# Optimization experiments

Measured on AMD Instinct MI355X. Metric: run time of the kernel, lower is better.

## Reference

```python
import jax, jax.numpy as jnp
import numpy as np
from jax import lax

H = 256          # hidden_size
VOCAB = 30000
N_OPS = 9
N_COLS = 16
T = 4            # num_time_steps
Q = 64           # question length
N_NUM = 8        # numbers appearing in the question
ROWS = 1_000_000

# operation indices (Neural Programmer, ICLR 2016 op set)
OP_SUM, OP_COUNT, OP_DIFF, OP_GREATER, OP_LESSER, OP_AND, OP_OR, OP_ASSIGN, OP_RESET = range(N_OPS)


def setup_inputs() -> dict:
    key = jax.random.key(0)
    ks = jax.random.split(key, 13)
    s = 0.05
    f32 = jnp.float32
    return {
        "input_question": jax.random.randint(ks[0], (Q,), 0, VOCAB),
        "input_question_numbers": jax.random.randint(ks[1], (N_NUM,), 0, 100),
        "left_word_indices": jax.random.randint(ks[2], (N_NUM,), 0, Q),
        "table": jax.random.normal(ks[3], (ROWS, N_COLS), f32),
        # learned parameters
        "emb": jax.random.normal(ks[4], (VOCAB, H), f32) * s,      # question word embeddings
        "Wx": jax.random.normal(ks[5], (H, H), f32) * s,           # question RNN input weight
        "Wh": jax.random.normal(ks[6], (H, H), f32) * s,           # question RNN recurrent weight
        "W_op": jax.random.normal(ks[7], (H, 2 * H), f32) * s,     # selector (op branch)
        "op_emb": jax.random.normal(ks[8], (N_OPS, H), f32) * s,   # operation embeddings
        "W_col": jax.random.normal(ks[9], (H, 2 * H), f32) * s,    # selector (column branch)
        "col_emb": jax.random.normal(ks[10], (N_COLS, H), f32) * s,# column embeddings
        "W_hist": jax.random.normal(ks[11], (H, 3 * H), f32) * s,  # history RNN
        "U": jax.random.normal(ks[12], (2, H), f32) * s,           # lesser/greater pivot vectors
    }


def reference(input_question, input_question_numbers, left_word_indices, table,
              emb, Wx, Wh, W_op, op_emb, W_col, col_emb, W_hist, U):
    dt = table.dtype
    hid = Wx.shape[0]

    # ---- question RNN (simple tanh RNN) ----
    xs = emb[input_question]                               # [Q, H]
    def step(h, x):
        h2 = jnp.tanh(x @ Wx.T + h @ Wh.T)
        return h2, h2
    q, hs = lax.scan(step, jnp.zeros((hid,), dt), xs)      # q=[H], hs=[Q,H]

    # ---- pivot computation (z_matrix = hidden states left of each number) ----
    z = hs[left_word_indices]                              # [N_NUM, H]
    nums = input_question_numbers.astype(dt)               # [N_NUM]
    l_pivot = jax.nn.softmax(z @ U[0]) @ nums              # scalar
    g_pivot = jax.nn.softmax(z @ U[1]) @ nums              # scalar

    # soft comparison maps (pivots are timestep-independent; compute once)
    sel_l = jax.nn.sigmoid(l_pivot - table)                # [R, C] ~ [table < l_pivot]
    sel_g = jax.nn.sigmoid(table - g_pivot)                # [R, C] ~ [table > g_pivot]

    h_hist = jnp.zeros((hid,), dt)
    scalars = [jnp.zeros((), dt)]
    rs_list = [jnp.ones((table.shape[0],), dt)]
    lookup = jnp.zeros(table.shape, dt)

    for _ in range(T):
        rs1 = rs_list[-1]
        rs2 = rs_list[max(0, len(rs_list) - 2)]
        s1 = scalars[-1]
        s3 = scalars[max(0, len(scalars) - 3)]

        # selector: soft op / column distributions from [question; history]
        qh = jnp.concatenate([q, h_hist])                  # [2H]
        a_op = jax.nn.softmax(op_emb @ jnp.tanh(W_op @ qh))    # [N_OPS]
        a_col = jax.nn.softmax(col_emb @ jnp.tanh(W_col @ qh)) # [N_COLS]

        # row select (soft mixture over ops)
        rs = (a_op[OP_GREATER] * (sel_g @ a_col)
              + a_op[OP_LESSER] * (sel_l @ a_col)
              + a_op[OP_AND] * jnp.minimum(rs1, rs2)
              + a_op[OP_OR] * jnp.maximum(rs1, rs2)
              + a_op[OP_RESET] * jnp.ones_like(rs1)
              + (a_op[OP_SUM] + a_op[OP_COUNT] + a_op[OP_DIFF] + a_op[OP_ASSIGN]) * rs1)

        # scalar answer
        scalar = (a_op[OP_SUM] * jnp.sum(rs1 @ table)
                  + a_op[OP_COUNT] * jnp.sum(rs1)
                  + a_op[OP_DIFF] * (s3 - s1))

        # lookup answer: assign op prints selected rows/columns
        lookup = a_op[OP_ASSIGN] * rs[:, None] * a_col[None, :]

        # history RNN
        c = jnp.concatenate([a_op @ op_emb, a_col @ col_emb, h_hist])  # [3H]
        h_hist = jnp.tanh(W_hist @ c)

        rs_list.append(rs)
        scalars.append(scalar)

    return scalars[-1], lookup
```

## Files before the change

### kernel.cpp

```cpp
#include <hip/hip_runtime.h>
#include <hip/hip_fp16.h>
#include <math.h>

#define HDIM   256
#define QLEN   64
#define NNUM   8
#define NOPS   9
#define NCOLS  16
#define TSTEPS 4


#define WS_LPIV 0
#define WS_GPIV 1
#define WS_ACOL 2
#define WS_AOP  66
#define WS_Q    112
#define WS_PQO  368
#define WS_PQC  624
#define WS_HS   880
#define WS_XP   2928
#define WS_AH   19312
#define WS_BH   21616
#define WS_WH16 25712
#define WS_M16  58480
#define WS_PART 156784
#define NBLK_C  2048
#define PRE2_BLOCKS 409

typedef _Float16 f16x8 __attribute__((ext_vector_type(8)));
typedef _Float16 f16x4 __attribute__((ext_vector_type(4)));
typedef float    f32x4 __attribute__((ext_vector_type(4)));

__device__ __forceinline__ float fast_tanh(float x) {
    return 1.0f - 2.0f / (__expf(2.0f * x) + 1.0f);
}

__global__ void precompute_kernel(const int* __restrict__ q,
                                  const float* __restrict__ emb,
                                  const float* __restrict__ Wx,
                                  const float* __restrict__ Wh,
                                  float* __restrict__ ws) {
    int gid = blockIdx.x * 256 + threadIdx.x;
    if (gid < QLEN * HDIM) {
        int t = gid >> 8, j = gid & 255;
        const float4* x4 = (const float4*)(emb + (size_t)q[t] * HDIM);
        const float4* w4 = (const float4*)(Wx + (size_t)j * HDIM);
        float s = 0.f;
        for (int k = 0; k < HDIM / 4; k++) {
            float4 a = x4[k], b = w4[k];
            s += a.x * b.x + a.y * b.y + a.z * b.z + a.w * b.w;
        }
        ws[WS_XP + t * HDIM + j] = s;
    } else {
        int did = gid - QLEN * HDIM;
        int hidx = did * 2;
        int e = hidx & 7, qr = (hidx >> 3) & 15, quad = (hidx >> 7) & 3;
        int kk = (hidx >> 9) & 7, t = hidx >> 12;
        const float* src = Wh + (size_t)(16 * t + qr) * HDIM + kk * 32 + quad * 8 + e;
        float2 v = *(const float2*)src;
        ((__half2*)(ws + WS_WH16))[did] = __floats2half2_rn(v.x, v.y);
    }
}

__global__ __launch_bounds__(256, 1) void rnn_kernel(
        float* __restrict__ ws,
        const int* __restrict__ lwi,
        const float* __restrict__ W_op,
        const float* __restrict__ W_col,
        const float* __restrict__ W_hist,
        const float* __restrict__ op_emb,
        const float* __restrict__ col_emb,
        const float* __restrict__ table,
        int rows) {
    if (blockIdx.x >= 1 + PRE2_BLOCKS) {
        int wid = blockIdx.x - 1 - PRE2_BLOCKS;
        const f32x4* t4 = (const f32x4*)table;
        long n4 = (long)rows * (NCOLS / 4);
        f32x4 acc = {0.f, 0.f, 0.f, 0.f};
        for (long i = (long)wid * 256 + threadIdx.x; i < n4; i += (long)2048 * 256)
            acc += t4[i];
        asm volatile("" :: "v"(acc));
        return;
    }
    if (blockIdx.x != 0) {
        int gid = (blockIdx.x - 1) * 256 + threadIdx.x;
        if (gid < HDIM * NOPS) {
            int j = gid / NOPS, o = gid % NOPS;
            const float4* w4 = (const float4*)(W_hist + (size_t)j * (3 * HDIM));
            const float4* e4 = (const float4*)(op_emb + (size_t)o * HDIM);
            float s = 0.f;
            for (int k = 0; k < HDIM / 4; k++) {
                float4 a = w4[k], b = e4[k];
                s += a.x * b.x + a.y * b.y + a.z * b.z + a.w * b.w;
            }
            ws[WS_AH + gid] = s;
        } else if (gid < HDIM * NOPS + HDIM * NCOLS) {
            int idx = gid - HDIM * NOPS;
            int j = idx / NCOLS, c = idx % NCOLS;
            const float4* w4 = (const float4*)(W_hist + (size_t)j * (3 * HDIM) + HDIM);
            const float4* e4 = (const float4*)(col_emb + (size_t)c * HDIM);
            float s = 0.f;
            for (int k = 0; k < HDIM / 4; k++) {
                float4 a = w4[k], b = e4[k];
                s += a.x * b.x + a.y * b.y + a.z * b.z + a.w * b.w;
            }
            ws[WS_BH + idx] = s;
        } else if (gid < HDIM * NOPS + HDIM * NCOLS + 98304) {
            int did = gid - (HDIM * NOPS + HDIM * NCOLS);
            int mat = did >> 15;
            int hidx = (did & 32767) * 2;
            int e = hidx & 7, j = (hidx >> 3) & 255, i = hidx >> 11;
            const float* src;
            if (mat == 0)      src = W_op   + (size_t)j * (2 * HDIM) + HDIM     + i * 8 + e;
            else if (mat == 1) src = W_col  + (size_t)j * (2 * HDIM) + HDIM     + i * 8 + e;
            else               src = W_hist + (size_t)j * (3 * HDIM) + 2 * HDIM + i * 8 + e;
            float2 v = *(const float2*)src;
            ((__half2*)(ws + WS_M16))[did] = __floats2half2_rn(v.x, v.y);
        }
        return;
    }

    __shared__ float xpL[QLEN * HDIM];
    __shared__ _Float16 hF[2][HDIM];
    __shared__ unsigned stepmask[QLEN];

    const int tid = threadIdx.x;
    const int wave = tid >> 6, lane = tid & 63;
    const int quad = lane >> 4, qr = lane & 15;
    const int myrow = 64 * wave + 16 * (qr >> 2) + quad * 4 + (qr & 3);

    #pragma unroll
    for (int i = 0; i < 16; i++) {
        int idx = (i * 256 + tid) * 4;
        *(float4*)(xpL + idx) = *(const float4*)(ws + WS_XP + idx);
    }
    if (tid < QLEN) {
        unsigned m = 0;
        #pragma unroll
        for (int i = 0; i < NNUM; i++) m |= (lwi[i] == tid) ? (1u << i) : 0u;
        stepmask[tid] = m;
    }
    const _Float16* wsh = (const _Float16*)(ws + WS_WH16);
    f16x8 aW[4][8];
    #pragma unroll
    for (int r = 0; r < 4; r++)
        #pragma unroll
        for (int kk = 0; kk < 8; kk++)
            aW[r][kk] = *(const f16x8*)(wsh + ((size_t)(((4 * wave + r) * 8 + kk) * 64 + lane)) * 8);
    #pragma unroll
    for (int r = 0; r < 4; r++)
        #pragma unroll
        for (int kk = 0; kk < 8; kk++) {
            f32x4 t = __builtin_bit_cast(f32x4, aW[r][kk]);
            asm volatile("" : "+v"(t));
            aW[r][kk] = __builtin_bit_cast(f16x8, t);
        }
    hF[0][tid] = (_Float16)0.f;
    __syncthreads();

    for (int s = 0; s < QLEN; s++) {
        const _Float16* hb = hF[s & 1];
        f16x8 bfrag[8];
        #pragma unroll
        for (int kk = 0; kk < 8; kk++)
            bfrag[kk] = *(const f16x8*)(hb + kk * 32 + quad * 8);
        f32x4 acc[4];
        #pragma unroll
        for (int r = 0; r < 4; r++) acc[r] = (f32x4){0.f, 0.f, 0.f, 0.f};
        #pragma unroll
        for (int kk = 0; kk < 8; kk++)
            #pragma unroll
            for (int r = 0; r < 4; r++)
                acc[r] = __builtin_amdgcn_mfma_f32_16x16x32_f16(aW[r][kk], bfrag[kk], acc[r], 0, 0, 0);

        f32x4 t01 = (qr & 4) ? acc[1] : acc[0];
        f32x4 t23 = (qr & 4) ? acc[3] : acc[2];
        f32x4 tt  = (qr & 8) ? t23 : t01;
        float e01 = (qr & 1) ? tt.y : tt.x;
        float e23 = (qr & 1) ? tt.w : tt.z;
        float v   = (qr & 2) ? e23 : e01;

        float h = fast_tanh(v + xpL[s * HDIM + myrow]);
        hF[(s + 1) & 1][myrow] = (_Float16)h;
        unsigned m = stepmask[s];
        while (m) {
            int i = __builtin_ctz(m);
            ws[WS_HS + i * HDIM + myrow] = h;
            m &= m - 1;
        }
        if (s == QLEN - 1) ws[WS_Q + myrow] = h;
        __syncthreads();
    }
}

__global__ void qproj_kernel(const float* __restrict__ W_op,
                             const float* __restrict__ W_col,
                             float* __restrict__ ws) {
    int gid = blockIdx.x * 256 + threadIdx.x;
    int dot = gid >> 5, l = gid & 31;
    int mat = dot >> 8, j = dot & 255;
    const float* w = (mat ? W_col : W_op) + (size_t)j * (2 * HDIM) + l * 8;
    const float* qv = ws + WS_Q + l * 8;
    float4 a0 = *(const float4*)w,        a1 = *(const float4*)(w + 4);
    float4 b0 = *(const float4*)qv,       b1 = *(const float4*)(qv + 4);
    float s = a0.x * b0.x + a0.y * b0.y + a0.z * b0.z + a0.w * b0.w
            + a1.x * b1.x + a1.y * b1.y + a1.z * b1.z + a1.w * b1.w;
    s += __shfl_xor(s, 1); s += __shfl_xor(s, 2); s += __shfl_xor(s, 4);
    s += __shfl_xor(s, 8); s += __shfl_xor(s, 16);
    if (l == 0) ws[(mat ? WS_PQC : WS_PQO) + j] = s;
}

__global__ __launch_bounds__(256) void select_kernel(
        float* __restrict__ ws,
        const float* __restrict__ U,
        const int* __restrict__ nums,
        const float* __restrict__ op_emb,
        const float* __restrict__ col_emb) {
    __shared__ float zu[16];
    __shared__ float hH[HDIM];
    __shared__ float top_op[HDIM], top_col[HDIM], mh[HDIM];
    __shared__ float logits[32];
    __shared__ float aop_s[NOPS], acol_s[NCOLS];

    const int tid = threadIdx.x;

    {
        int g = tid >> 4, l = tid & 15;
        int i = g >> 1, u = g & 1;
        const float* z = ws + WS_HS + i * HDIM + l * 16;
        const float* uu = U + u * HDIM + l * 16;
        float s = 0.f;
        #pragma unroll
        for (int k = 0; k < 4; k++) {
            float4 a = *(const float4*)(z + k * 4), b = *(const float4*)(uu + k * 4);
            s += a.x * b.x + a.y * b.y + a.z * b.z + a.w * b.w;
        }
        s += __shfl_xor(s, 1); s += __shfl_xor(s, 2);
        s += __shfl_xor(s, 4); s += __shfl_xor(s, 8);
        if (l == 0) zu[g] = s;
    }
    if (tid < HDIM) hH[tid] = 0.f;
    __syncthreads();
    if (tid == 0) {
        #pragma unroll
        for (int u = 0; u < 2; u++) {
            float mx = -1e30f;
            for (int i = 0; i < NNUM; i++) mx = fmaxf(mx, zu[i * 2 + u]);
            float se = 0.f, pv = 0.f;
            for (int i = 0; i < NNUM; i++) {
                float e = __expf(zu[i * 2 + u] - mx);
                se += e;
                pv += e * (float)nums[i];
            }
            ws[u] = pv / se;
        }
    }
    __syncthreads();

    const _Float16* wsm = (const _Float16*)(ws + WS_M16);
    const float pqo = ws[WS_PQO + tid];
    const float pqc = ws[WS_PQC + tid];

    for (int t = 0; t < TSTEPS; t++) {
        float so = 0.f, sc = 0.f, sh = 0.f;
        #pragma unroll
        for (int i = 0; i < 32; i++) {
            float4 h0 = *(const float4*)(hH + i * 8);
            float4 h1 = *(const float4*)(hH + i * 8 + 4);
            f16x8 a = *(const f16x8*)(wsm + ((size_t)(0 * 32 + i) * 256 + tid) * 8);
            f16x8 b = *(const f16x8*)(wsm + ((size_t)(1 * 32 + i) * 256 + tid) * 8);
            f16x8 c = *(const f16x8*)(wsm + ((size_t)(2 * 32 + i) * 256 + tid) * 8);
            so += (float)a[0]*h0.x + (float)a[1]*h0.y + (float)a[2]*h0.z + (float)a[3]*h0.w
                + (float)a[4]*h1.x + (float)a[5]*h1.y + (float)a[6]*h1.z + (float)a[7]*h1.w;
            sc += (float)b[0]*h0.x + (float)b[1]*h0.y + (float)b[2]*h0.z + (float)b[3]*h0.w
                + (float)b[4]*h1.x + (float)b[5]*h1.y + (float)b[6]*h1.z + (float)b[7]*h1.w;
            sh += (float)c[0]*h0.x + (float)c[1]*h0.y + (float)c[2]*h0.z + (float)c[3]*h0.w
                + (float)c[4]*h1.x + (float)c[5]*h1.y + (float)c[6]*h1.z + (float)c[7]*h1.w;
        }
        top_op[tid]  = fast_tanh(pqo + so);
        top_col[tid] = fast_tanh(pqc + sc);
        mh[tid] = sh;
        __syncthreads();

        #pragma unroll
        for (int d0 = 0; d0 < 32; d0 += 8) {
            int d = d0 + (tid >> 5), l = tid & 31;
            if (d < 25) {
                float s = 0.f;
                if (d < NOPS) {
                    const float* e = op_emb + (size_t)d * HDIM;
                    #pragma unroll
                    for (int m = 0; m < 8; m++) s += e[l * 8 + m] * top_op[l * 8 + m];
                } else {
                    const float* e = col_emb + (size_t)(d - NOPS) * HDIM;
                    #pragma unroll
                    for (int m = 0; m < 8; m++) s += e[l * 8 + m] * top_col[l * 8 + m];
                }
                s += __shfl_xor(s, 1); s += __shfl_xor(s, 2); s += __shfl_xor(s, 4);
                s += __shfl_xor(s, 8); s += __shfl_xor(s, 16);
                if (l == 0) logits[d] = s;
            }
        }
        __syncthreads();
        if (tid == 0) {
            float mx = -1e30f;
            for (int o = 0; o < NOPS; o++) mx = fmaxf(mx, logits[o]);
            float se = 0.f, e[NOPS];
            for (int o = 0; o < NOPS; o++) { e[o] = __expf(logits[o] - mx); se += e[o]; }
            for (int o = 0; o < NOPS; o++) {
                float a = e[o] / se;
                aop_s[o] = a;
                ws[WS_AOP + t * NOPS + o] = a;
            }
        } else if (tid == 32) {
            float mx = -1e30f;
            for (int c = 0; c < NCOLS; c++) mx = fmaxf(mx, logits[NOPS + c]);
            float se = 0.f, e[NCOLS];
            for (int c = 0; c < NCOLS; c++) { e[c] = __expf(logits[NOPS + c] - mx); se += e[c]; }
            for (int c = 0; c < NCOLS; c++) {
                float a = e[c] / se;
                acol_s[c] = a;
                ws[WS_ACOL + t * NCOLS + c] = a;
            }
        }
        __syncthreads();
        {
            float s = mh[tid];
            const float* ah = ws + WS_AH + tid * NOPS;
            #pragma unroll
            for (int o = 0; o < NOPS; o++) s += ah[o] * aop_s[o];
            const float* bh = ws + WS_BH + tid * NCOLS;
            #pragma unroll
            for (int c = 0; c < NCOLS; c++) s += bh[c] * acol_s[c];
            float hv = fast_tanh(s);
            __syncthreads();
            hH[tid] = hv;
        }
        __syncthreads();
    }
}

__global__ __launch_bounds__(256) void table_kernel(
        const float* __restrict__ table,
        const float* __restrict__ wsc,
        float* __restrict__ wspart,
        float* __restrict__ out,
        int rows) {
    const int tid = threadIdx.x;
    const int cq = tid & 3;
    const float lpiv = wsc[WS_LPIV];
    const float gpiv = wsc[WS_GPIV];
    float4 acol4[TSTEPS];
    float wg[TSTEPS], wl[TSTEPS], wand[TSTEPS], wor[TSTEPS], wrst[TSTEPS], wpass[TSTEPS];
    #pragma unroll
    for (int t = 0; t < TSTEPS; t++) {
        acol4[t] = make_float4(wsc[WS_ACOL + t * NCOLS + cq * 4 + 0],
                               wsc[WS_ACOL + t * NCOLS + cq * 4 + 1],
                               wsc[WS_ACOL + t * NCOLS + cq * 4 + 2],
                               wsc[WS_ACOL + t * NCOLS + cq * 4 + 3]);
        wg[t]   = wsc[WS_AOP + t * NOPS + 3];
        wl[t]   = wsc[WS_AOP + t * NOPS + 4];
        wand[t] = wsc[WS_AOP + t * NOPS + 5];
        wor[t]  = wsc[WS_AOP + t * NOPS + 6];
        wrst[t] = wsc[WS_AOP + t * NOPS + 8];
        wpass[t] = wsc[WS_AOP + t * NOPS + 0] + wsc[WS_AOP + t * NOPS + 1]
                 + wsc[WS_AOP + t * NOPS + 2] + wsc[WS_AOP + t * NOPS + 7];
    }
    const float wassign = wsc[WS_AOP + 3 * NOPS + 7];

    float dAcc[TSTEPS] = {0.f, 0.f, 0.f, 0.f};
    float nAcc[TSTEPS] = {0.f, 0.f, 0.f, 0.f};
    const long rowsL = rows;

    for (long r0 = (long)blockIdx.x * 64; r0 < rowsL; r0 += (long)NBLK_C * 64) {
        long row = r0 + (tid >> 2);
        bool valid = row < rowsL;
        f32x4 tv = {0.f, 0.f, 0.f, 0.f};
        if (valid)
            tv = __builtin_nontemporal_load((const f32x4*)(table + row * NCOLS + cq * 4));
        float prs = tv.x + tv.y + tv.z + tv.w;
        float pg[4], pl[4];
        {
            float c0 = tv.x, c1 = tv.y, c2 = tv.z, c3 = tv.w;
            float sg0 = __builtin_amdgcn_rcpf(1.f + __expf(gpiv - c0));
            float sg1 = __builtin_amdgcn_rcpf(1.f + __expf(gpiv - c1));
            float sg2 = __builtin_amdgcn_rcpf(1.f + __expf(gpiv - c2));
            float sg3 = __builtin_amdgcn_rcpf(1.f + __expf(gpiv - c3));
            float sl0 = __builtin_amdgcn_rcpf(1.f + __expf(c0 - lpiv));
            float sl1 = __builtin_amdgcn_rcpf(1.f + __expf(c1 - lpiv));
            float sl2 = __builtin_amdgcn_rcpf(1.f + __expf(c2 - lpiv));
            float sl3 = __builtin_amdgcn_rcpf(1.f + __expf(c3 - lpiv));
            #pragma unroll
            for (int t = 0; t < TSTEPS; t++) {
                pg[t] = sg0 * acol4[t].x + sg1 * acol4[t].y + sg2 * acol4[t].z + sg3 * acol4[t].w;
                pl[t] = sl0 * acol4[t].x + sl1 * acol4[t].y + sl2 * acol4[t].z + sl3 * acol4[t].w;
            }
        }
        prs += __shfl_xor(prs, 1); prs += __shfl_xor(prs, 2);
        #pragma unroll
        for (int t = 0; t < TSTEPS; t++) {
            pg[t] += __shfl_xor(pg[t], 1); pg[t] += __shfl_xor(pg[t], 2);
            pl[t] += __shfl_xor(pl[t], 1); pl[t] += __shfl_xor(pl[t], 2);
        }
        float rs1 = 1.f, rs2 = 1.f;
        float vf = valid ? 1.f : 0.f;
        #pragma unroll
        for (int i = 0; i < TSTEPS; i++) {
            dAcc[i] += vf * rs1 * prs;
            nAcc[i] += vf * rs1;
            float nrs = wg[i] * pg[i] + wl[i] * pl[i]
                      + wand[i] * fminf(rs1, rs2) + wor[i] * fmaxf(rs1, rs2)
                      + wrst[i] + wpass[i] * rs1;
            rs2 = rs1;
            rs1 = nrs;
        }
        if (valid) {
            float wa = wassign * rs1;
            float* ob = out + 1 + row * NCOLS + cq * 4;
            ob[0] = wa * acol4[3].x;
            ob[1] = wa * acol4[3].y;
            ob[2] = wa * acol4[3].z;
            ob[3] = wa * acol4[3].w;
        }
    }

    #pragma unroll
    for (int i = 0; i < TSTEPS; i++) {
        #pragma unroll
        for (int off = 32; off >= 1; off >>= 1) {
            dAcc[i] += __shfl_xor(dAcc[i], off);
            nAcc[i] += __shfl_xor(nAcc[i], off);
        }
    }
    __shared__ float redl[4][8];
    int wv = tid >> 6, ln = tid & 63;
    if (ln == 0) {
        #pragma unroll
        for (int i = 0; i < TSTEPS; i++) {
            redl[wv][i] = dAcc[i];
            redl[wv][4 + i] = nAcc[i];
        }
    }
    __syncthreads();
    if (tid < 8) {
        float s = redl[0][tid] + redl[1][tid] + redl[2][tid] + redl[3][tid];
        wspart[blockIdx.x * 8 + tid] = 0.25f * s;
    }
}

__global__ void finalize_kernel(const float* __restrict__ ws, float* __restrict__ out) {
    __shared__ float red[8];
    int a = threadIdx.x >> 5, l = threadIdx.x & 31;
    float s = 0.f;
    for (int b = l; b < NBLK_C; b += 32) s += ws[WS_PART + b * 8 + a];
    s += __shfl_xor(s, 1, 32); s += __shfl_xor(s, 2, 32); s += __shfl_xor(s, 4, 32);
    s += __shfl_xor(s, 8, 32); s += __shfl_xor(s, 16, 32);
    if (l == 0) red[a] = s;
    __syncthreads();
    if (threadIdx.x == 0) {
        float Dv[4] = {red[0], red[1], red[2], red[3]};
        float Nv[4] = {red[4], red[5], red[6], red[7]};
        const float* aop = ws + WS_AOP;
        float sc[5];
        sc[0] = 0.f;
        #pragma unroll
        for (int i = 0; i < 4; i++) {
            float s1 = sc[i];
            float s3 = sc[(i >= 2) ? (i - 2) : 0];
            sc[i + 1] = aop[i * NOPS + 0] * Dv[i] + aop[i * NOPS + 1] * Nv[i]
                      + aop[i * NOPS + 2] * (s3 - s1);
        }
        out[0] = sc[4];
    }
}

extern "C" void kernel_launch(void* const* d_in, const int* in_sizes, int n_in,
                              void* d_out, int out_size, void* d_ws, size_t ws_size,
                              hipStream_t stream) {
    const int*   q       = (const int*)d_in[0];
    const int*   nums    = (const int*)d_in[1];
    const int*   lwi     = (const int*)d_in[2];
    const float* table   = (const float*)d_in[3];
    const float* emb     = (const float*)d_in[4];
    const float* Wx      = (const float*)d_in[5];
    const float* Wh      = (const float*)d_in[6];
    const float* W_op    = (const float*)d_in[7];
    const float* op_emb  = (const float*)d_in[8];
    const float* W_col   = (const float*)d_in[9];
    const float* col_emb = (const float*)d_in[10];
    const float* W_hist  = (const float*)d_in[11];
    const float* U       = (const float*)d_in[12];
    float* out = (float*)d_out;
    float* ws  = (float*)d_ws;
    int rows = in_sizes[3] / NCOLS;

    precompute_kernel<<<192, 256, 0, stream>>>(q, emb, Wx, Wh, ws);
    rnn_kernel<<<1 + PRE2_BLOCKS + 2048, 256, 0, stream>>>(
        ws, lwi, W_op, W_col, W_hist, op_emb, col_emb, table, rows);
    qproj_kernel<<<64, 256, 0, stream>>>(W_op, W_col, ws);
    select_kernel<<<1, 256, 0, stream>>>(ws, U, nums, op_emb, col_emb);
    table_kernel<<<NBLK_C, 256, 0, stream>>>(
        table, ws, ws + WS_PART, out, rows);
    finalize_kernel<<<1, 256, 0, stream>>>(ws, out);
}
```

Before: 259.4 us.

## Fuse finalize into table kernel, split RNN MFMA chain, drop nontemporal load

Three changes. The separate finalize launch is removed: each table block stores its partials atomically, and the last block to increment an atomic counter does the final reduction and scalar computation. The RNN step's MFMA accumulation is split into two independent accumulator chains to shorten the dependency chain on the serial critical path. The table load is switched from nontemporal to a normal load. Together these cut one kernel launch and some recurrent latency, in exchange for an atomic counter that must be reset each call and possibly different cache behaviour when streaming the table.

```diff
diff --git a/kernel.cpp b/kernel.cpp
--- a/kernel.cpp
+++ b/kernel.cpp
@@ -24,6 +24,7 @@
 #define WS_WH16 25712
 #define WS_M16  58480
 #define WS_PART 156784
+#define WS_CNT  173168
 #define NBLK_C  2048
 #define PRE2_BLOCKS 409
 
@@ -41,6 +42,7 @@
                                   const float* __restrict__ Wh,
                                   float* __restrict__ ws) {
     int gid = blockIdx.x * 256 + threadIdx.x;
+    if (gid == 0) *(unsigned*)(ws + WS_CNT) = 0u;
     if (gid < QLEN * HDIM) {
         int t = gid >> 8, j = gid & 255;
         const float4* x4 = (const float4*)(emb + (size_t)q[t] * HDIM);
@@ -164,14 +166,24 @@
         #pragma unroll
         for (int kk = 0; kk < 8; kk++)
             bfrag[kk] = *(const f16x8*)(hb + kk * 32 + quad * 8);
-        f32x4 acc[4];
-        #pragma unroll
-        for (int r = 0; r < 4; r++) acc[r] = (f32x4){0.f, 0.f, 0.f, 0.f};
-        #pragma unroll
-        for (int kk = 0; kk < 8; kk++)
+        f32x4 acc[4], accB[4];
+        #pragma unroll
+        for (int r = 0; r < 4; r++) {
+            acc[r]  = (f32x4){0.f, 0.f, 0.f, 0.f};
+            accB[r] = (f32x4){0.f, 0.f, 0.f, 0.f};
+        }
+        #pragma unroll
+        for (int kk = 0; kk < 4; kk++)
             #pragma unroll
             for (int r = 0; r < 4; r++)
                 acc[r] = __builtin_amdgcn_mfma_f32_16x16x32_f16(aW[r][kk], bfrag[kk], acc[r], 0, 0, 0);
+        #pragma unroll
+        for (int kk = 4; kk < 8; kk++)
+            #pragma unroll
+            for (int r = 0; r < 4; r++)
+                accB[r] = __builtin_amdgcn_mfma_f32_16x16x32_f16(aW[r][kk], bfrag[kk], accB[r], 0, 0, 0);
+        #pragma unroll
+        for (int r = 0; r < 4; r++) acc[r] += accB[r];
 
         f32x4 t01 = (qr & 4) ? acc[1] : acc[0];
         f32x4 t23 = (qr & 4) ? acc[3] : acc[2];
@@ -377,7 +389,7 @@
         bool valid = row < rowsL;
         f32x4 tv = {0.f, 0.f, 0.f, 0.f};
         if (valid)
-            tv = __builtin_nontemporal_load((const f32x4*)(table + row * NCOLS + cq * 4));
+            tv = *(const f32x4*)(table + row * NCOLS + cq * 4);
         float prs = tv.x + tv.y + tv.z + tv.w;
         float pg[4], pl[4];
         {
@@ -444,33 +456,45 @@
     __syncthreads();
     if (tid < 8) {
         float s = redl[0][tid] + redl[1][tid] + redl[2][tid] + redl[3][tid];
-        wspart[blockIdx.x * 8 + tid] = 0.25f * s;
-    }
-}
-
-__global__ void finalize_kernel(const float* __restrict__ ws, float* __restrict__ out) {
-    __shared__ float red[8];
-    int a = threadIdx.x >> 5, l = threadIdx.x & 31;
-    float s = 0.f;
-    for (int b = l; b < NBLK_C; b += 32) s += ws[WS_PART + b * 8 + a];
-    s += __shfl_xor(s, 1, 32); s += __shfl_xor(s, 2, 32); s += __shfl_xor(s, 4, 32);
-    s += __shfl_xor(s, 8, 32); s += __shfl_xor(s, 16, 32);
-    if (l == 0) red[a] = s;
+        __hip_atomic_store(&wspart[blockIdx.x * 8 + tid], 0.25f * s,
+                           __ATOMIC_RELAXED, __HIP_MEMORY_SCOPE_AGENT);
+    }
     __syncthreads();
-    if (threadIdx.x == 0) {
-        float Dv[4] = {red[0], red[1], red[2], red[3]};
-        float Nv[4] = {red[4], red[5], red[6], red[7]};
-        const float* aop = ws + WS_AOP;
-        float sc[5];
-        sc[0] = 0.f;
-        #pragma unroll
-        for (int i = 0; i < 4; i++) {
-            float s1 = sc[i];
-            float s3 = sc[(i >= 2) ? (i - 2) : 0];
-            sc[i + 1] = aop[i * NOPS + 0] * Dv[i] + aop[i * NOPS + 1] * Nv[i]
-                      + aop[i * NOPS + 2] * (s3 - s1);
-        }
-        out[0] = sc[4];
+
+    __shared__ int lastFlag;
+    if (tid == 0) {
+        unsigned* cnt = (unsigned*)(wspart + NBLK_C * 8);
+        unsigned old = __hip_atomic_fetch_add(cnt, 1u, __ATOMIC_ACQ_REL,
+                                              __HIP_MEMORY_SCOPE_AGENT);
+        lastFlag = (old == NBLK_C - 1) ? 1 : 0;
+    }
+    __syncthreads();
+    if (lastFlag) {
+        __shared__ float redF[8];
+        int a = tid >> 5, l = tid & 31;
+        float s = 0.f;
+        for (int b = l; b < NBLK_C; b += 32)
+            s += __hip_atomic_load(&wspart[b * 8 + a], __ATOMIC_RELAXED,
+                                   __HIP_MEMORY_SCOPE_AGENT);
+        s += __shfl_xor(s, 1, 32); s += __shfl_xor(s, 2, 32); s += __shfl_xor(s, 4, 32);
+        s += __shfl_xor(s, 8, 32); s += __shfl_xor(s, 16, 32);
+        if (l == 0) redF[a] = s;
+        __syncthreads();
+        if (tid == 0) {
+            float Dv[4] = {redF[0], redF[1], redF[2], redF[3]};
+            float Nv[4] = {redF[4], redF[5], redF[6], redF[7]};
+            const float* aop = wsc + WS_AOP;
+            float sc[5];
+            sc[0] = 0.f;
+            #pragma unroll
+            for (int i = 0; i < 4; i++) {
+                float s1 = sc[i];
+                float s3 = sc[(i >= 2) ? (i - 2) : 0];
+                sc[i + 1] = aop[i * NOPS + 0] * Dv[i] + aop[i * NOPS + 1] * Nv[i]
+                          + aop[i * NOPS + 2] * (s3 - s1);
+            }
+            out[0] = sc[4];
+        }
     }
 }
 
@@ -501,5 +525,4 @@
     select_kernel<<<1, 256, 0, stream>>>(ws, U, nums, op_emb, col_emb);
     table_kernel<<<NBLK_C, 256, 0, stream>>>(
         table, ws, ws + WS_PART, out, rows);
-    finalize_kernel<<<1, 256, 0, stream>>>(ws, out);
-}
+}
```

After: 335.5 us. 29.4% more time.
